# Kernel optimization log

Hardware: AMD Instinct MI355X
Metric: run time of the kernel (lower is better)

Reference implementation:

```python
import jax, jax.numpy as jnp
import numpy as np

N = 256   # units (waveguides)
L = 256   # num_layers (rectangular mesh: L == N)
B = 16384 # batch
TWO_PI = 2.0 * np.pi


def _perm_indices():
    # Rectangular-mesh column permutations: alternate +/-1 circular shifts so
    # successive columns couple (0,1),(2,3),... then (1,2),(3,4),...; final
    # permutation undoes the net shift (perm_layers has L+1 entries).
    ar = np.arange(N)
    shifts = [0] + [(1 if l % 2 == 1 else -1) for l in range(1, L)]
    perms = [(ar + s) % N for s in shifts]
    perms.append((ar - sum(shifts)) % N)
    return np.asarray(perms, dtype=np.int32)  # (L+1, N)


def setup_inputs() -> dict:
    key = jax.random.key(0)
    ks = jax.random.split(key, 5)
    x_re = jax.random.normal(ks[0], (B, N), jnp.float32)
    x_im = jax.random.normal(ks[1], (B, N), jnp.float32)
    theta = jax.random.uniform(ks[2], (L, N // 2), jnp.float32) * TWO_PI
    phi = jax.random.uniform(ks[3], (L, N // 2), jnp.float32) * TWO_PI
    gamma = jax.random.uniform(ks[4], (N,), jnp.float32) * TWO_PI
    perm_idx = jnp.asarray(_perm_indices())
    pp = np.arange(N).reshape(-1, 2)[:, ::-1].reshape(-1)  # [1,0,3,2,...]
    pairwise_perm_idx = jnp.asarray(pp, dtype=jnp.int32)
    return dict(x_re=x_re, x_im=x_im, theta=theta, phi=phi, gamma=gamma,
                perm_idx=perm_idx, pairwise_perm_idx=pairwise_perm_idx)


def _mesh_diag_offdiag(theta, phi):
    # Bloch basis, differential internal arrangement: +theta/2 on top port
    # (even waveguide), -theta/2 on bottom port (odd waveguide).
    t = theta.T  # (N/2, L)
    internal = jnp.stack([t * 0.5, -t * 0.5], axis=1).reshape(N, L)
    # single-mode external arrangement: phi on top port, 0 on bottom.
    external = jnp.stack([phi.T, jnp.zeros_like(phi.T)], axis=1).reshape(N, L)
    ipsl = jnp.exp(1j * internal)   # (N, L) complex64
    epsl = jnp.exp(1j * external)
    up = lambda a: jnp.roll(a, -1, axis=0)   # roll_tensor(x, up=True)
    dn = lambda a: jnp.roll(a, 1, axis=0)    # roll_tensor(x)
    e = jnp.float32(0.5)  # ideal 50:50 splitters -> all mzi_error_tensors = 0.5
    # hadamard = False branch of Mesh.mesh_layers
    s11 = e * ipsl - e * up(ipsl)
    s22 = dn(-e * ipsl + e * up(ipsl))
    s12 = 1j * dn(e * ipsl + e * up(ipsl))
    s21 = 1j * (e * ipsl + e * up(ipsl))
    diag = epsl * (s11 + s22) * 0.5
    off = dn(epsl) * (s21 + s12) * 0.5
    return diag.T, off.T  # (L, N)


def reference(x_re, x_im, theta, phi, gamma, perm_idx, pairwise_perm_idx):
    diag, off = _mesh_diag_offdiag(theta, phi)
    # include_diagonal_phases: input phase screen exp(i*gamma)
    x = (x_re + 1j * x_im) * jnp.exp(1j * gamma)[None, :]

    def step(x, lay):
        perm, d, o = lay
        x = jnp.take(x, perm, axis=-1)                              # PermutationLayer
        x = x * d + jnp.take(x * o, pairwise_perm_idx, axis=-1)     # MZI couple
        return x, None

    x, _ = jax.lax.scan(step, x, (perm_idx[:L], diag, off))
    x = jnp.take(x, perm_idx[L], axis=-1)  # right_perm of final layer
    return jnp.stack([jnp.real(x), jnp.imag(x)])  # (2, B, N) float32
```

## Files before the change

### kernel.cpp

```cpp
#include <hip/hip_runtime.h>
#include <math.h>

#define NN 256
#define LL 256
#define BB 16384

typedef __attribute__((ext_vector_type(8))) short short8;
typedef __attribute__((ext_vector_type(4))) float f32x4;


__global__ __launch_bounds__(256) void coefF_kernel(const float* __restrict__ theta,
                                                    const float* __restrict__ phi,
                                                    const float* __restrict__ gamma,
                                                    float4* __restrict__ coef) {
    __shared__ double ipc[128], ips[128], epc[128], eps[128];
    const int l = blockIdx.x;
    const int t = threadIdx.x;
    if (t < 128) {
        double s, c;
        sincos((double)theta[l * 128 + t] * 0.5, &s, &c); ipc[t] = c; ips[t] = s;
        sincos((double)phi[l * 128 + t], &s, &c);         epc[t] = c; eps[t] = s;
    }
    __syncthreads();

    const int j = t;
    const int u = l & 1;
    const int n = (j - u) & 255;
    const int m = n ^ 1;

    auto ipsl = [&](int k, double& re, double& im) {
        k &= 255;
        re = ipc[k >> 1];
        im = (k & 1) ? -ips[k >> 1] : ips[k >> 1];
    };
    double inr, ini, ipr, ipi, imr, imi;
    ipsl(n, inr, ini); ipsl(n + 1, ipr, ipi); ipsl(n - 1, imr, imi);
    double enr = 1.0, eni = 0.0;
    if (!(n & 1)) { enr = epc[n >> 1]; eni = eps[n >> 1]; }
    double dr = 2.0 * inr - ipr - imr;
    double di = 2.0 * ini - ipi - imi;
    double Dre = 0.25 * (enr * dr - eni * di);
    double Dim = 0.25 * (enr * di + eni * dr);
    ipsl(m, inr, ini); ipsl(m + 1, ipr, ipi); ipsl(m - 1, imr, imi);
    int mm = (m - 1) & 255;
    double emr = 1.0, emi = 0.0;
    if (!(mm & 1)) { emr = epc[mm >> 1]; emi = eps[mm >> 1]; }
    double orv = 2.0 * inr + ipr + imr;
    double oiv = 2.0 * ini + ipi + imi;
    double tre = emr * orv - emi * oiv;
    double tim = emr * oiv + emi * orv;
    double Ore = -0.25 * tim;
    double Oim =  0.25 * tre;

    if (l == 0) {
        double s, c;
        sincos((double)gamma[j], &s, &c);
        double a2 = Dre * c - Dim * s, b2 = Dre * s + Dim * c;
        Dre = a2; Dim = b2;
        sincos((double)gamma[j ^ 1], &s, &c);
        a2 = Ore * c - Oim * s; b2 = Ore * s + Oim * c;
        Ore = a2; Oim = b2;
    }
    coef[l * 256 + (j & 7) * 32 + (j >> 3)] =
        make_float4((float)Dre, (float)Dim, (float)Ore, (float)Oim);
}

__device__ __forceinline__ float2 mzi(float2 cD, float2 cO, float2 y, float2 p) {
    float2 t;
    asm("v_pk_mul_f32 %0, %1, %2 op_sel:[1,1] op_sel_hi:[1,0] neg_lo:[1,0]"
        : "=v"(t) : "v"(cO), "v"(p));
    asm("v_pk_fma_f32 %0, %1, %2, %0 op_sel:[0,0,0] op_sel_hi:[0,1,1]"
        : "+v"(t) : "v"(cO), "v"(p));
    asm("v_pk_fma_f32 %0, %1, %2, %0 op_sel:[1,1,0] op_sel_hi:[1,0,1] neg_lo:[1,0,0]"
        : "+v"(t) : "v"(cD), "v"(y));
    asm("v_pk_fma_f32 %0, %1, %2, %0 op_sel:[0,0,0] op_sel_hi:[0,1,1]"
        : "+v"(t) : "v"(cD), "v"(y));
    return t;
}
__device__ __forceinline__ float2 D_(float4 c) { return make_float2(c.x, c.y); }
__device__ __forceinline__ float2 O_(float4 c) { return make_float2(c.z, c.w); }

__global__ __launch_bounds__(256) void prop_kernel(const float4* __restrict__ coef,
                                                   float2* __restrict__ PA,
                                                   float2* __restrict__ PB) {
    const int lane = threadIdx.x & 63;
    const int wave = threadIdx.x >> 6;
    const int l32  = lane & 31;
    const int half = lane >> 5;
    const int gid  = blockIdx.x * 4 + wave;
    const int mhalf = gid >> 6;
    const int c4   = (gid & 63) * 4;
    const int l0   = mhalf ? 128 : 0;
    const int idxL4 = (((lane & 32) | ((lane - 1) & 31))) << 2;
    const int idxR4 = (((lane & 32) | ((lane + 1) & 31))) << 2;

    float2 y[2][8];
#pragma unroll
    for (int s2 = 0; s2 < 2; ++s2) {
        int row = c4 + 2 * s2 + half;
#pragma unroll
        for (int j = 0; j < 8; ++j)
            y[s2][j] = make_float2((8 * l32 + j == row) ? 1.f : 0.f, 0.f);
    }

    const float4* cp = coef + l32;
    auto loadl = [&](int l, float4& c0, float4& c1, float4& c2, float4& c3,
                            float4& c4_, float4& c5, float4& c6, float4& c7) {
        const float4* p = cp + l * 256;
        c0 = p[0 * 32]; c1 = p[1 * 32]; c2 = p[2 * 32]; c3 = p[3 * 32];
        c4_ = p[4 * 32]; c5 = p[5 * 32]; c6 = p[6 * 32]; c7 = p[7 * 32];
    };

    float4 a0, a1, a2, a3, a4, a5, a6, a7;
    float4 b0, b1, b2, b3, b4, b5, b6, b7;
    loadl(l0, a0, a1, a2, a3, a4, a5, a6, a7);

#pragma unroll 1
    for (int it = 0; it < 64; ++it) {
        loadl(l0 + 2 * it + 1, b0, b1, b2, b3, b4, b5, b6, b7);
#pragma unroll
        for (int s2 = 0; s2 < 2; ++s2) {
            float2 t0 = y[s2][0], t1 = y[s2][1], t2 = y[s2][2], t3 = y[s2][3];
            float2 t4 = y[s2][4], t5 = y[s2][5], t6 = y[s2][6], t7 = y[s2][7];
            y[s2][0] = mzi(D_(a0), O_(a0), t0, t1);
            y[s2][1] = mzi(D_(a1), O_(a1), t1, t0);
            y[s2][2] = mzi(D_(a2), O_(a2), t2, t3);
            y[s2][3] = mzi(D_(a3), O_(a3), t3, t2);
            y[s2][4] = mzi(D_(a4), O_(a4), t4, t5);
            y[s2][5] = mzi(D_(a5), O_(a5), t5, t4);
            y[s2][6] = mzi(D_(a6), O_(a6), t6, t7);
            y[s2][7] = mzi(D_(a7), O_(a7), t7, t6);
        }
        if (it < 63) loadl(l0 + 2 * it + 2, a0, a1, a2, a3, a4, a5, a6, a7);
#pragma unroll
        for (int s2 = 0; s2 < 2; ++s2) {
            float2 t0 = y[s2][0], t1 = y[s2][1], t2 = y[s2][2], t3 = y[s2][3];
            float2 t4 = y[s2][4], t5 = y[s2][5], t6 = y[s2][6], t7 = y[s2][7];
            float2 plo, phi2;
            plo.x  = __int_as_float(__builtin_amdgcn_ds_bpermute(idxL4, __float_as_int(t7.x)));
            plo.y  = __int_as_float(__builtin_amdgcn_ds_bpermute(idxL4, __float_as_int(t7.y)));
            phi2.x = __int_as_float(__builtin_amdgcn_ds_bpermute(idxR4, __float_as_int(t0.x)));
            phi2.y = __int_as_float(__builtin_amdgcn_ds_bpermute(idxR4, __float_as_int(t0.y)));
            y[s2][1] = mzi(D_(b1), O_(b1), t1, t2);
            y[s2][2] = mzi(D_(b2), O_(b2), t2, t1);
            y[s2][3] = mzi(D_(b3), O_(b3), t3, t4);
            y[s2][4] = mzi(D_(b4), O_(b4), t4, t3);
            y[s2][5] = mzi(D_(b5), O_(b5), t5, t6);
            y[s2][6] = mzi(D_(b6), O_(b6), t6, t5);
            y[s2][0] = mzi(D_(b0), O_(b0), t0, plo);
            y[s2][7] = mzi(D_(b7), O_(b7), t7, phi2);
        }
    }

    float2* P = mhalf ? PB : PA;
#pragma unroll
    for (int s2 = 0; s2 < 2; ++s2) {
        int row = c4 + 2 * s2 + half;
#pragma unroll
        for (int j = 0; j < 8; ++j)
            P[row * 256 + 8 * l32 + j] = y[s2][j];
    }
}

__device__ __forceinline__ unsigned short bf16rne(float f) {
    unsigned int u2 = __float_as_uint(f);
    unsigned int r = (u2 + 0x7FFFu + ((u2 >> 16) & 1u)) >> 16;
    return (unsigned short)r;
}
__device__ __forceinline__ float bf16f(unsigned short h) {
    return __uint_as_float(((unsigned int)h) << 16);
}
__device__ __forceinline__ void split3(float v, unsigned short& h0,
                                       unsigned short& h1, unsigned short& h2) {
    h0 = bf16rne(v);        float r1 = v - bf16f(h0);
    h1 = bf16rne(r1);       float r2 = r1 - bf16f(h1);
    h2 = bf16rne(r2);
}

__global__ __launch_bounds__(256) void combineW_kernel(const float2* __restrict__ PA,
                                                       const float2* __restrict__ PB,
                                                       unsigned short* __restrict__ Wt) {
    int i = blockIdx.x, j = threadIdx.x;
    float accr = 0.f, acci = 0.f;
#pragma unroll 8
    for (int k = 0; k < 256; ++k) {
        float2 a = PA[i * 256 + k];
        float2 b = PB[k * 256 + j];
        accr += a.x * b.x - a.y * b.y;
        acci += a.x * b.y + a.y * b.x;
    }
    unsigned short r0, r1, r2, i0, i1, i2, n0, n1, n2;
    split3(accr, r0, r1, r2);
    split3(acci, i0, i1, i2);
    split3(-acci, n0, n1, n2);
    unsigned short* W0 = Wt;
    unsigned short* W1 = Wt + 262144;
    unsigned short* W2 = Wt + 524288;
    W0[j * 512 + i] = r0;           W1[j * 512 + i] = r1;           W2[j * 512 + i] = r2;
    W0[(j + 256) * 512 + i] = i0;   W1[(j + 256) * 512 + i] = i1;   W2[(j + 256) * 512 + i] = i2;
    W0[j * 512 + i + 256] = n0;     W1[j * 512 + i + 256] = n1;     W2[j * 512 + i + 256] = n2;
    W0[(j + 256) * 512 + i + 256] = r0;
    W1[(j + 256) * 512 + i + 256] = r1;
    W2[(j + 256) * 512 + i + 256] = r2;
}

__global__ __launch_bounds__(256, 2) void gemm_kernel(
        const float* __restrict__ x_re, const float* __restrict__ x_im,
        const unsigned short* __restrict__ Wt, float* __restrict__ out) {
    __shared__ unsigned short XL[3][128][40];
    __shared__ unsigned short WL[3][128][40];

    const int t    = threadIdx.x;
    const int lane = t & 63;
    const int wave = t >> 6;
    const int wm   = wave >> 1, wn = wave & 1;
    const int nt = blockIdx.x & 3, mt = blockIdx.x >> 2;
    const int m0 = mt * 128, n0 = nt * 128;
    const int lr = lane & 15, lg = lane >> 4;

    f32x4 acc[4][4];
#pragma unroll
    for (int a = 0; a < 4; ++a)
#pragma unroll
        for (int b = 0; b < 4; ++b) acc[a][b] = (f32x4)0.f;

#pragma unroll 1
    for (int ks = 0; ks < 16; ++ks) {
        const int k0 = ks * 32;
        const float* xsrc = (k0 < 256) ? x_re : x_im;
        const int kcol = k0 & 255;
#pragma unroll
        for (int r = 0; r < 4; ++r) {
            int F = r * 256 + t;
            int row = F >> 3, g = F & 7;
            float4 v = ((const float4*)xsrc)[(m0 + row) * 64 + (kcol >> 2) + g];
            unsigned short h0[4], h1[4], h2[4];
            split3(v.x, h0[0], h1[0], h2[0]);
            split3(v.y, h0[1], h1[1], h2[1]);
            split3(v.z, h0[2], h1[2], h2[2]);
            split3(v.w, h0[3], h1[3], h2[3]);
            *(ushort4*)&XL[0][row][g * 4] = make_ushort4(h0[0], h0[1], h0[2], h0[3]);
            *(ushort4*)&XL[1][row][g * 4] = make_ushort4(h1[0], h1[1], h1[2], h1[3]);
            *(ushort4*)&XL[2][row][g * 4] = make_ushort4(h2[0], h2[1], h2[2], h2[3]);
        }
#pragma unroll
        for (int r = 0; r < 6; ++r) {
            int U = r * 256 + t;
            int p = U >> 9, rem = U & 511;
            int n = rem >> 2, ku = (rem & 3) * 8;
            uint4 v = ((const uint4*)Wt)[p * 32768 + (n0 + n) * 64 + ((k0 + ku) >> 3)];
            *(uint4*)&WL[p][n][ku] = v;
        }
        __syncthreads();

        short8 bfr[3][4];
#pragma unroll
        for (int p = 0; p < 3; ++p)
#pragma unroll
            for (int ni = 0; ni < 4; ++ni)
                bfr[p][ni] = *(const short8*)&WL[p][wn * 64 + ni * 16 + lr][lg * 8];

#pragma unroll
        for (int i = 0; i < 3; ++i) {
            short8 af[4];
#pragma unroll
            for (int mi = 0; mi < 4; ++mi)
                af[mi] = *(const short8*)&XL[i][wm * 64 + mi * 16 + lr][lg * 8];
#pragma unroll
            for (int jj = 0; jj < 3; ++jj) {
                if (i + jj > 2) continue;
#pragma unroll
                for (int mi = 0; mi < 4; ++mi)
#pragma unroll
                    for (int ni = 0; ni < 4; ++ni)
                        acc[mi][ni] = __builtin_amdgcn_mfma_f32_16x16x32_bf16(
                            af[mi], bfr[jj][ni], acc[mi][ni], 0, 0, 0);
            }
        }
        __syncthreads();
    }

#pragma unroll
    for (int mi = 0; mi < 4; ++mi) {
#pragma unroll
        for (int ni = 0; ni < 4; ++ni) {
            int nglob = n0 + wn * 64 + ni * 16 + lr;
            float* dst = (nglob < 256)
                       ? out + (size_t)nglob
                       : out + (size_t)BB * 256 + (nglob - 256);
#pragma unroll
            for (int e = 0; e < 4; ++e) {
                int m = m0 + wm * 64 + mi * 16 + lg * 4 + e;
                dst[(size_t)m * 256] = acc[mi][ni][e];
            }
        }
    }
}

extern "C" void kernel_launch(void* const* d_in, const int* in_sizes, int n_in,
                              void* d_out, int out_size, void* d_ws, size_t ws_size,
                              hipStream_t stream) {
    const float* x_re  = (const float*)d_in[0];
    const float* x_im  = (const float*)d_in[1];
    const float* theta = (const float*)d_in[2];
    const float* phi   = (const float*)d_in[3];
    const float* gamma = (const float*)d_in[4];

    char* ws = (char*)d_ws;
    float4* coef        = (float4*)ws;
    float2* PA          = (float2*)(ws + (1 << 20));
    float2* PB          = (float2*)(ws + (1 << 20) + (512 << 10));
    unsigned short* Wt  = (unsigned short*)(ws + (2 << 20));

    hipLaunchKernelGGL(coefF_kernel, dim3(256), dim3(256), 0, stream,
                       theta, phi, gamma, coef);
    hipLaunchKernelGGL(prop_kernel, dim3(32), dim3(256), 0, stream, coef, PA, PB);
    hipLaunchKernelGGL(combineW_kernel, dim3(256), dim3(256), 0, stream, PA, PB, Wt);
    hipLaunchKernelGGL(gemm_kernel, dim3(512), dim3(256), 0, stream,
                       x_re, x_im, Wt, (float*)d_out);
}
```

Baseline: 198.8 us.

## Split mesh propagation into layer chunks and combine with tree matmuls

The sequential propagation of identity columns through the mesh is split into 8 chunks of 32 layers instead of 2 chunks of 128, and each wave now carries one row instead of two. The launch grows from 32 to 256 blocks, which shortens the serial dependency chain and fills more compute units. The chunk transfer matrices are then multiplied pairwise in two new tree_kernel passes, with combineW doing the last product. combineW now computes 4 rows per block so each B load is reused. The cost is two extra kernel launches and extra complex matmul work, plus more intermediate workspace traffic.

```diff
diff --git a/kernel.cpp b/kernel.cpp
--- a/kernel.cpp
+++ b/kernel.cpp
@@ -81,34 +81,29 @@
 __device__ __forceinline__ float2 O_(float4 c) { return make_float2(c.z, c.w); }
 
 __global__ __launch_bounds__(256) void prop_kernel(const float4* __restrict__ coef,
-                                                   float2* __restrict__ PA,
-                                                   float2* __restrict__ PB) {
+                                                   float2* __restrict__ Pbase) {
     const int lane = threadIdx.x & 63;
     const int wave = threadIdx.x >> 6;
     const int l32  = lane & 31;
     const int half = lane >> 5;
     const int gid  = blockIdx.x * 4 + wave;
-    const int mhalf = gid >> 6;
-    const int c4   = (gid & 63) * 4;
-    const int l0   = mhalf ? 128 : 0;
+    const int chunk = gid >> 7;
+    const int row  = ((gid & 127) << 1) | half;
+    const int l0   = chunk * 32;
     const int idxL4 = (((lane & 32) | ((lane - 1) & 31))) << 2;
     const int idxR4 = (((lane & 32) | ((lane + 1) & 31))) << 2;
 
-    float2 y[2][8];
-#pragma unroll
-    for (int s2 = 0; s2 < 2; ++s2) {
-        int row = c4 + 2 * s2 + half;
-#pragma unroll
-        for (int j = 0; j < 8; ++j)
-            y[s2][j] = make_float2((8 * l32 + j == row) ? 1.f : 0.f, 0.f);
-    }
+    float2 y[8];
+#pragma unroll
+    for (int j = 0; j < 8; ++j)
+        y[j] = make_float2((8 * l32 + j == row) ? 1.f : 0.f, 0.f);
 
     const float4* cp = coef + l32;
     auto loadl = [&](int l, float4& c0, float4& c1, float4& c2, float4& c3,
-                            float4& c4_, float4& c5, float4& c6, float4& c7) {
+                            float4& c4, float4& c5, float4& c6, float4& c7) {
         const float4* p = cp + l * 256;
         c0 = p[0 * 32]; c1 = p[1 * 32]; c2 = p[2 * 32]; c3 = p[3 * 32];
-        c4_ = p[4 * 32]; c5 = p[5 * 32]; c6 = p[6 * 32]; c7 = p[7 * 32];
+        c4 = p[4 * 32]; c5 = p[5 * 32]; c6 = p[6 * 32]; c7 = p[7 * 32];
     };
 
     float4 a0, a1, a2, a3, a4, a5, a6, a7;
@@ -116,50 +111,73 @@
     loadl(l0, a0, a1, a2, a3, a4, a5, a6, a7);
 
 #pragma unroll 1
-    for (int it = 0; it < 64; ++it) {
+    for (int it = 0; it < 16; ++it) {
         loadl(l0 + 2 * it + 1, b0, b1, b2, b3, b4, b5, b6, b7);
-#pragma unroll
-        for (int s2 = 0; s2 < 2; ++s2) {
-            float2 t0 = y[s2][0], t1 = y[s2][1], t2 = y[s2][2], t3 = y[s2][3];
-            float2 t4 = y[s2][4], t5 = y[s2][5], t6 = y[s2][6], t7 = y[s2][7];
-            y[s2][0] = mzi(D_(a0), O_(a0), t0, t1);
-            y[s2][1] = mzi(D_(a1), O_(a1), t1, t0);
-            y[s2][2] = mzi(D_(a2), O_(a2), t2, t3);
-            y[s2][3] = mzi(D_(a3), O_(a3), t3, t2);
-            y[s2][4] = mzi(D_(a4), O_(a4), t4, t5);
-            y[s2][5] = mzi(D_(a5), O_(a5), t5, t4);
-            y[s2][6] = mzi(D_(a6), O_(a6), t6, t7);
-            y[s2][7] = mzi(D_(a7), O_(a7), t7, t6);
-        }
-        if (it < 63) loadl(l0 + 2 * it + 2, a0, a1, a2, a3, a4, a5, a6, a7);
-#pragma unroll
-        for (int s2 = 0; s2 < 2; ++s2) {
-            float2 t0 = y[s2][0], t1 = y[s2][1], t2 = y[s2][2], t3 = y[s2][3];
-            float2 t4 = y[s2][4], t5 = y[s2][5], t6 = y[s2][6], t7 = y[s2][7];
+        {
+            float2 t0 = y[0], t1 = y[1], t2 = y[2], t3 = y[3];
+            float2 t4 = y[4], t5 = y[5], t6 = y[6], t7 = y[7];
+            y[0] = mzi(D_(a0), O_(a0), t0, t1);
+            y[1] = mzi(D_(a1), O_(a1), t1, t0);
+            y[2] = mzi(D_(a2), O_(a2), t2, t3);
+            y[3] = mzi(D_(a3), O_(a3), t3, t2);
+            y[4] = mzi(D_(a4), O_(a4), t4, t5);
+            y[5] = mzi(D_(a5), O_(a5), t5, t4);
+            y[6] = mzi(D_(a6), O_(a6), t6, t7);
+            y[7] = mzi(D_(a7), O_(a7), t7, t6);
+        }
+        if (it < 15) loadl(l0 + 2 * it + 2, a0, a1, a2, a3, a4, a5, a6, a7);
+        {
+            float2 t0 = y[0], t1 = y[1], t2 = y[2], t3 = y[3];
+            float2 t4 = y[4], t5 = y[5], t6 = y[6], t7 = y[7];
             float2 plo, phi2;
             plo.x  = __int_as_float(__builtin_amdgcn_ds_bpermute(idxL4, __float_as_int(t7.x)));
             plo.y  = __int_as_float(__builtin_amdgcn_ds_bpermute(idxL4, __float_as_int(t7.y)));
             phi2.x = __int_as_float(__builtin_amdgcn_ds_bpermute(idxR4, __float_as_int(t0.x)));
             phi2.y = __int_as_float(__builtin_amdgcn_ds_bpermute(idxR4, __float_as_int(t0.y)));
-            y[s2][1] = mzi(D_(b1), O_(b1), t1, t2);
-            y[s2][2] = mzi(D_(b2), O_(b2), t2, t1);
-            y[s2][3] = mzi(D_(b3), O_(b3), t3, t4);
-            y[s2][4] = mzi(D_(b4), O_(b4), t4, t3);
-            y[s2][5] = mzi(D_(b5), O_(b5), t5, t6);
-            y[s2][6] = mzi(D_(b6), O_(b6), t6, t5);
-            y[s2][0] = mzi(D_(b0), O_(b0), t0, plo);
-            y[s2][7] = mzi(D_(b7), O_(b7), t7, phi2);
-        }
-    }
-
-    float2* P = mhalf ? PB : PA;
-#pragma unroll
-    for (int s2 = 0; s2 < 2; ++s2) {
-        int row = c4 + 2 * s2 + half;
-#pragma unroll
-        for (int j = 0; j < 8; ++j)
-            P[row * 256 + 8 * l32 + j] = y[s2][j];
-    }
+            y[1] = mzi(D_(b1), O_(b1), t1, t2);
+            y[2] = mzi(D_(b2), O_(b2), t2, t1);
+            y[3] = mzi(D_(b3), O_(b3), t3, t4);
+            y[4] = mzi(D_(b4), O_(b4), t4, t3);
+            y[5] = mzi(D_(b5), O_(b5), t5, t6);
+            y[6] = mzi(D_(b6), O_(b6), t6, t5);
+            y[0] = mzi(D_(b0), O_(b0), t0, plo);
+            y[7] = mzi(D_(b7), O_(b7), t7, phi2);
+        }
+    }
+
+    float2* P = Pbase + chunk * 65536;
+#pragma unroll
+    for (int j = 0; j < 8; ++j)
+        P[row * 256 + 8 * l32 + j] = y[j];
+}
+
+__global__ __launch_bounds__(256) void tree_kernel(const float2* __restrict__ base,
+                                                   float2* __restrict__ outb) {
+    const int mat = blockIdx.x >> 6;
+    const int i0  = (blockIdx.x & 63) * 4;
+    const int j   = threadIdx.x;
+    const float2* A = base + mat * 131072;
+    const float2* B = A + 65536;
+    float2* C = outb + mat * 65536;
+
+    float acr0 = 0.f, aci0 = 0.f, acr1 = 0.f, aci1 = 0.f;
+    float acr2 = 0.f, aci2 = 0.f, acr3 = 0.f, aci3 = 0.f;
+#pragma unroll 8
+    for (int k = 0; k < 256; ++k) {
+        float2 b = B[k * 256 + j];
+        float2 a0 = A[(i0 + 0) * 256 + k];
+        float2 a1 = A[(i0 + 1) * 256 + k];
+        float2 a2 = A[(i0 + 2) * 256 + k];
+        float2 a3 = A[(i0 + 3) * 256 + k];
+        acr0 += a0.x * b.x - a0.y * b.y;  aci0 += a0.x * b.y + a0.y * b.x;
+        acr1 += a1.x * b.x - a1.y * b.y;  aci1 += a1.x * b.y + a1.y * b.x;
+        acr2 += a2.x * b.x - a2.y * b.y;  aci2 += a2.x * b.y + a2.y * b.x;
+        acr3 += a3.x * b.x - a3.y * b.y;  aci3 += a3.x * b.y + a3.y * b.x;
+    }
+    C[(i0 + 0) * 256 + j] = make_float2(acr0, aci0);
+    C[(i0 + 1) * 256 + j] = make_float2(acr1, aci1);
+    C[(i0 + 2) * 256 + j] = make_float2(acr2, aci2);
+    C[(i0 + 3) * 256 + j] = make_float2(acr3, aci3);
 }
 
 __device__ __forceinline__ unsigned short bf16rne(float f) {
@@ -177,31 +195,42 @@
     h2 = bf16rne(r2);
 }
 
-__global__ __launch_bounds__(256) void combineW_kernel(const float2* __restrict__ PA,
-                                                       const float2* __restrict__ PB,
+__global__ __launch_bounds__(256) void combineW_kernel(const float2* __restrict__ R,
                                                        unsigned short* __restrict__ Wt) {
-    int i = blockIdx.x, j = threadIdx.x;
-    float accr = 0.f, acci = 0.f;
+    const int i0 = blockIdx.x * 4;
+    const int j  = threadIdx.x;
+    const float2* A = R;
+    const float2* B = R + 65536;
+
+    float acr[4] = {0.f, 0.f, 0.f, 0.f};
+    float aci[4] = {0.f, 0.f, 0.f, 0.f};
 #pragma unroll 8
     for (int k = 0; k < 256; ++k) {
-        float2 a = PA[i * 256 + k];
-        float2 b = PB[k * 256 + j];
-        accr += a.x * b.x - a.y * b.y;
-        acci += a.x * b.y + a.y * b.x;
-    }
-    unsigned short r0, r1, r2, i0, i1, i2, n0, n1, n2;
-    split3(accr, r0, r1, r2);
-    split3(acci, i0, i1, i2);
-    split3(-acci, n0, n1, n2);
+        float2 b = B[k * 256 + j];
+#pragma unroll
+        for (int r = 0; r < 4; ++r) {
+            float2 a = A[(i0 + r) * 256 + k];
+            acr[r] += a.x * b.x - a.y * b.y;
+            aci[r] += a.x * b.y + a.y * b.x;
+        }
+    }
     unsigned short* W0 = Wt;
     unsigned short* W1 = Wt + 262144;
     unsigned short* W2 = Wt + 524288;
-    W0[j * 512 + i] = r0;           W1[j * 512 + i] = r1;           W2[j * 512 + i] = r2;
-    W0[(j + 256) * 512 + i] = i0;   W1[(j + 256) * 512 + i] = i1;   W2[(j + 256) * 512 + i] = i2;
-    W0[j * 512 + i + 256] = n0;     W1[j * 512 + i + 256] = n1;     W2[j * 512 + i + 256] = n2;
-    W0[(j + 256) * 512 + i + 256] = r0;
-    W1[(j + 256) * 512 + i + 256] = r1;
-    W2[(j + 256) * 512 + i + 256] = r2;
+#pragma unroll
+    for (int r = 0; r < 4; ++r) {
+        const int i = i0 + r;
+        unsigned short r0, r1, r2, i0s, i1s, i2s, n0, n1, n2;
+        split3(acr[r], r0, r1, r2);
+        split3(aci[r], i0s, i1s, i2s);
+        split3(-aci[r], n0, n1, n2);
+        W0[j * 512 + i] = r0;           W1[j * 512 + i] = r1;           W2[j * 512 + i] = r2;
+        W0[(j + 256) * 512 + i] = i0s;  W1[(j + 256) * 512 + i] = i1s;  W2[(j + 256) * 512 + i] = i2s;
+        W0[j * 512 + i + 256] = n0;     W1[j * 512 + i + 256] = n1;     W2[j * 512 + i + 256] = n2;
+        W0[(j + 256) * 512 + i + 256] = r0;
+        W1[(j + 256) * 512 + i + 256] = r1;
+        W2[(j + 256) * 512 + i + 256] = r2;
+    }
 }
 
 __global__ __launch_bounds__(256, 2) void gemm_kernel(
@@ -308,14 +337,17 @@
 
     char* ws = (char*)d_ws;
     float4* coef        = (float4*)ws;
-    float2* PA          = (float2*)(ws + (1 << 20));
-    float2* PB          = (float2*)(ws + (1 << 20) + (512 << 10));
+    float2* P           = (float2*)(ws + (1 << 20));
+    float2* Q           = (float2*)(ws + (5 << 20));
+    float2* R           = (float2*)(ws + (1 << 20));
     unsigned short* Wt  = (unsigned short*)(ws + (2 << 20));
 
     hipLaunchKernelGGL(coefF_kernel, dim3(256), dim3(256), 0, stream,
                        theta, phi, gamma, coef);
-    hipLaunchKernelGGL(prop_kernel, dim3(32), dim3(256), 0, stream, coef, PA, PB);
-    hipLaunchKernelGGL(combineW_kernel, dim3(256), dim3(256), 0, stream, PA, PB, Wt);
+    hipLaunchKernelGGL(prop_kernel, dim3(256), dim3(256), 0, stream, coef, P);
+    hipLaunchKernelGGL(tree_kernel, dim3(256), dim3(256), 0, stream, P, Q);
+    hipLaunchKernelGGL(tree_kernel, dim3(128), dim3(256), 0, stream, Q, R);
+    hipLaunchKernelGGL(combineW_kernel, dim3(64), dim3(256), 0, stream, R, Wt);
     hipLaunchKernelGGL(gemm_kernel, dim3(512), dim3(256), 0, stream,
                        x_re, x_im, Wt, (float*)d_out);
 }
```

Measured after the change: 234.3 us. 17.9% more time.
